# Performance work log

Hardware: AMD Instinct MI355X
Metric: run time of the kernel (lower is better)

Reference implementation:

```python
import jax, jax.numpy as jnp
import numpy as np

C = 256
G = 32            # GroupNorm groups = min(32, C)
DQK = C // 8      # q/k channel dim
EPS = 1e-5


def setup_inputs() -> dict:
    key = jax.random.key(0)
    ks = jax.random.split(key, 10)
    B, H, W = 4, 64, 64
    s = 0.02
    return {
        "x": jax.random.normal(ks[0], (B, C, H, W), dtype=jnp.float32),
        "gamma": jnp.ones((C,), jnp.float32),
        "beta": jnp.zeros((C,), jnp.float32),
        "wq": jax.random.normal(ks[1], (DQK, C), jnp.float32) * s,
        "bq": jnp.zeros((DQK,), jnp.float32),
        "wk": jax.random.normal(ks[2], (DQK, C), jnp.float32) * s,
        "bk": jnp.zeros((DQK,), jnp.float32),
        "wv": jax.random.normal(ks[3], (C, C), jnp.float32) * s,
        "bv": jnp.zeros((C,), jnp.float32),
        "wp": jax.random.normal(ks[4], (C, C), jnp.float32) * s,
        "bp": jnpp if False else jnp.zeros((C,), jnp.float32),
    }


def reference(x, gamma, beta, wq, bq, wk, bk, wv, bv, wp, bp):
    B, Cc, H, W = x.shape
    N = H * W
    # GroupNorm(32, C), affine
    h = x.reshape(B, G, Cc // G, H, W)
    mu = h.mean(axis=(2, 3, 4), keepdims=True)
    var = h.var(axis=(2, 3, 4), keepdims=True)
    h = (h - mu) * jax.lax.rsqrt(var + EPS)
    h = h.reshape(B, Cc, N) * gamma[:, None] + beta[:, None]
    # 1x1 convs == per-token linear maps over channels
    q = jnp.einsum('dc,bcn->bnd', wq, h) + bq            # [B, N, DQK]
    k = jnp.einsum('dc,bcn->bdn', wk, h) + bk[:, None]   # [B, DQK, N]
    v = jnp.einsum('ec,bcn->ben', wv, h) + bv[:, None]   # [B, C, N]
    scale = DQK ** (-0.5)
    attn = jax.nn.softmax(jnp.einsum('bnd,bdm->bnm', q, k) * scale, axis=-1)
    out = jnp.einsum('bnm,bem->ben', attn, v)            # [B, C, N]
    proj = jnp.einsum('fe,ben->bfn', wp, out) + bp[:, None]
    return x + proj.reshape(B, Cc, H, W)
```

## Files before the change

### kernel.cpp

```cpp
#include <hip/hip_runtime.h>
#include <hip/hip_bf16.h>

#define NB 4
#define CD 256
#define NT 4096
#define DQ 32

typedef __attribute__((ext_vector_type(8))) __bf16 bf16x8;
typedef __attribute__((ext_vector_type(16))) float float16v;
typedef __attribute__((ext_vector_type(4))) unsigned int uint4v;
typedef __attribute__((ext_vector_type(2))) unsigned int uint2v;

#if __has_builtin(__builtin_amdgcn_exp2f)
#define EXP2(x) __builtin_amdgcn_exp2f(x)
#else
#define EXP2(x) exp2f(x)
#endif

__device__ inline unsigned short f2bf(float f) {
  unsigned u = __float_as_uint(f);
  u += 0x7fffu + ((u >> 16) & 1u);
  return (unsigned short)(u >> 16);
}

#define BARRIER() asm volatile("s_waitcnt lgkmcnt(0)\n\ts_barrier" ::: "memory")

__global__ __launch_bounds__(1024) void gn_fused(
    const float* __restrict__ x, const float* __restrict__ gamma,
    const float* __restrict__ beta, const float* __restrict__ wq,
    const float* __restrict__ wk, const float* __restrict__ wv,
    const float* __restrict__ wp, const float* __restrict__ bq,
    const float* __restrict__ bk, const float* __restrict__ bv,
    unsigned short* __restrict__ h, unsigned short* __restrict__ wqkv,
    unsigned short* __restrict__ wpb, float* __restrict__ bias) {
  int bx = blockIdx.x;
  int tid = threadIdx.x;
  if (bx < 128) {
    int b = bx >> 5, g = bx & 31, c0 = g * 8;
    const float4* xp = (const float4*)(x + (size_t)bx * 32768);
    float va[32];
    float s = 0.f, ss = 0.f;
#pragma unroll
    for (int i = 0; i < 8; i++) {
      float4 t4 = xp[i * 1024 + tid];
      va[4 * i + 0] = t4.x;
      va[4 * i + 1] = t4.y;
      va[4 * i + 2] = t4.z;
      va[4 * i + 3] = t4.w;
      s += t4.x + t4.y + t4.z + t4.w;
      ss += t4.x * t4.x + t4.y * t4.y + t4.z * t4.z + t4.w * t4.w;
    }
#pragma unroll
    for (int off = 32; off >= 1; off >>= 1) {
      s += __shfl_xor(s, off);
      ss += __shfl_xor(ss, off);
    }
    __shared__ float red[32];
    int wid = tid >> 6;
    if ((tid & 63) == 0) {
      red[wid] = s;
      red[16 + wid] = ss;
    }
    __syncthreads();
    float S = 0.f, SS = 0.f;
#pragma unroll
    for (int i = 0; i < 16; i++) {
      S += red[i];
      SS += red[16 + i];
    }
    float mu = S * (1.f / 32768.f);
    float rstd = rsqrtf(SS * (1.f / 32768.f) - mu * mu + 1e-5f);
    float gam[8], bet[8];
#pragma unroll
    for (int i = 0; i < 8; i++) {
      gam[i] = gamma[c0 + i] * rstd;
      bet[i] = beta[c0 + i] - mu * gamma[c0 + i] * rstd;
    }
    unsigned short* hb = h + (size_t)b * NT * CD + c0;
#pragma unroll
    for (int j = 0; j < 4; j++) {
      unsigned short hv[8];
#pragma unroll
      for (int i = 0; i < 8; i++) {
        hv[i] = f2bf(va[4 * i + j] * gam[i] + bet[i]);
      }
      *(uint4v*)(hb + (size_t)(4 * tid + j) * CD) = *(uint4v*)hv;
    }
  } else {
    const float scale2 = 0.2550348909867343f;
    int i = (bx - 128) * 1024 + tid;
    if (i < 320 * 256) {
      int j = i >> 8, c = i & 255;
      float v;
      if (j < 32) v = wq[j * 256 + c] * scale2;
      else if (j < 64) v = wk[(j - 32) * 256 + c];
      else v = wv[(j - 64) * 256 + c];
      wqkv[i] = f2bf(v);
    } else if (i < 320 * 256 + 256 * 256) {
      int k = i - 320 * 256;
      wpb[k] = f2bf(wp[k]);
    } else if (i < 320 * 256 + 256 * 256 + 320) {
      int j = i - (320 * 256 + 256 * 256);
      float v;
      if (j < 32) v = bq[j] * scale2;
      else if (j < 64) v = bk[j - 32];
      else v = bv[j - 64];
      bias[j] = v;
    }
  }
}

__global__ __launch_bounds__(256) void qkv_gemm(
    const unsigned short* __restrict__ A, const unsigned short* __restrict__ H,
    const float* __restrict__ bias, unsigned short* __restrict__ qk,
    unsigned short* __restrict__ v) {
  int nt = blockIdx.x, mt = blockIdx.y, b = blockIdx.z;
  int tid = threadIdx.x, lane = tid & 63;
  int w = tid >> 6, mi = w & 1, ni = w >> 1;
  int l31 = lane & 31, hh = lane >> 5;
  int m_base = mt * 64 + 32 * mi;
  int n_base = nt * 128 + 64 * ni;
  const unsigned short* Arow = A + (size_t)(m_base + l31) * 256 + 8 * hh;
  const unsigned short* Hb = H + (size_t)b * NT * CD;
  const unsigned short* h0 = Hb + (size_t)(n_base + l31) * CD + 8 * hh;
  const unsigned short* h1 = h0 + (size_t)32 * CD;
  float16v acc0, acc1;
#pragma unroll
  for (int r = 0; r < 16; r++) { acc0[r] = 0.f; acc1[r] = 0.f; }
#pragma unroll
  for (int s = 0; s < 16; s++) {
    bf16x8 af = *(const bf16x8*)(Arow + 16 * s);
    bf16x8 b0 = *(const bf16x8*)(h0 + 16 * s);
    bf16x8 b1 = *(const bf16x8*)(h1 + 16 * s);
    acc0 = __builtin_amdgcn_mfma_f32_32x32x16_bf16(af, b0, acc0, 0, 0, 0);
    acc1 = __builtin_amdgcn_mfma_f32_32x32x16_bf16(af, b1, acc1, 0, 0, 0);
  }
  float bj[16];
  int jr[16];
#pragma unroll
  for (int r = 0; r < 16; r++) {
    jr[r] = m_base + (r & 3) + 8 * (r >> 2) + 4 * hh;
    bj[r] = bias[jr[r]];
  }
#pragma unroll
  for (int half = 0; half < 2; half++) {
    int n = n_base + 32 * half + l31;
#pragma unroll
    for (int r = 0; r < 16; r++) {
      float val = (half ? acc1[r] : acc0[r]) + bj[r];
      int j = jr[r];
      if (j < 64) {
        qk[((size_t)b * NT + n) * 64 + j] = f2bf(val);
      } else {
        int e = j - 64;
        int itg = n >> 6, sp = (n >> 4) & 3;
        int ls = ((n >> 3) & 1) * 32 + (e & 31);
        int el = n & 7, et = e >> 5;
        v[((((size_t)b * 64 + itg) * 8 + et) * 4 + sp) * 512 + ls * 8 + el] =
            f2bf(val);
      }
    }
  }
}

#define K_STAGE(PCUR)                                                         \
  if (tid >= 256) {                                                           \
    *(uint4v*)&Ks[(((PCUR) + 1) & 1) * 2304 + skr * 36 + skc] = kreg;         \
    int pk_ = (PCUR) + 2 <= 31 ? (PCUR) + 2 : 31;                             \
    kreg =                                                                    \
        *(const uint4v*)&qkb[(size_t)(mbase + pk_ * 64 + skr) * 64 + 32 + skc]; \
  }

#define QK_STEP(PCUR)                                                         \
  if (w < 4) {                                                                \
    float16v st;                                                              \
    _Pragma("unroll") for (int r = 0; r < 16; r++) st[r] = 0.f;               \
    __builtin_amdgcn_s_setprio(1);                                            \
    _Pragma("unroll") for (int s = 0; s < 2; s++) {                           \
      bf16x8 af = *(const bf16x8*)&Ks[((PCUR) & 1) * 2304 +                   \
                                      (32 * ks2 + l31) * 36 + 16 * s + 8 * hh]; \
      st = __builtin_amdgcn_mfma_f32_32x32x16_bf16(af, qfr[s], st, 0, 0, 0);  \
    }                                                                         \
    __builtin_amdgcn_s_setprio(0);                                            \
    _Pragma("unroll") for (int rq = 0; rq < 4; rq++) {                        \
      float e0 = EXP2(st[4 * rq + 0]);                                        \
      float e1 = EXP2(st[4 * rq + 1]);                                        \
      float e2 = EXP2(st[4 * rq + 2]);                                        \
      float e3 = EXP2(st[4 * rq + 3]);                                        \
      lsum += (e0 + e1) + (e2 + e3);                                          \
      uint2v pw;                                                              \
      pw[0] = __builtin_amdgcn_perm(__float_as_uint(e1), __float_as_uint(e0), \
                                    0x07060302u);                             \
      pw[1] = __builtin_amdgcn_perm(__float_as_uint(e3), __float_as_uint(e2), \
                                    0x07060302u);                             \
      *(uint2v*)&Pbuf[((PCUR) & 1) * 4352 + (qs * 32 + l31) * 68 + 8 * rq +   \
                      4 * hh + 32 * ks2] = pw;                                \
    }                                                                         \
  }

#define PV_STEP(PPREV, CURV)                                                  \
  {                                                                           \
    __builtin_amdgcn_s_setprio(1);                                            \
    _Pragma("unroll") for (int sp = 0; sp < 4; sp++) {                        \
      bf16x8 a0 = *(const bf16x8*)&Pbuf[((PPREV) & 1) * 4352 + l31 * 68 +     \
                                        16 * sp + 8 * hh];                    \
      bf16x8 a1 = *(const bf16x8*)&Pbuf[((PPREV) & 1) * 4352 +                \
                                        (32 + l31) * 68 + 16 * sp + 8 * hh];  \
      acc[0] = __builtin_amdgcn_mfma_f32_32x32x16_bf16(a0, CURV[sp], acc[0],  \
                                                       0, 0, 0);              \
      acc[1] = __builtin_amdgcn_mfma_f32_32x32x16_bf16(a1, CURV[sp], acc[1],  \
                                                       0, 0, 0);              \
    }                                                                         \
    __builtin_amdgcn_s_setprio(0);                                            \
  }

#define V_LOAD(DST, ITX)                                                      \
  {                                                                           \
    const unsigned short* vp_ = vbase + (size_t)(ITX)*16384;                  \
    _Pragma("unroll") for (int u = 0; u < 4; u++)                             \
        DST[u] = *(const bf16x8*)(vp_ + u * 512);                             \
  }

__global__ __launch_bounds__(512, 4) void attn_fused(
    const unsigned short* __restrict__ qk, const unsigned short* __restrict__ Vp,
    unsigned short* __restrict__ Pa, unsigned short* __restrict__ Pb,
    float* __restrict__ lp4) {
  int L = blockIdx.x;
  int xv = L & 7;
  int b = xv >> 1;
  int kh = xv & 1;
  int n0 = (L >> 3) * 64;
  int tid = threadIdx.x, lane = tid & 63, w = tid >> 6;
  int l31 = lane & 31, hh = lane >> 5;
  int qs = w & 1, ks2 = (w >> 1) & 1;

  __shared__ unsigned short Ks[2 * 2304];
  __shared__ unsigned short Pbuf[2 * 4352];

  const unsigned short* qkb = qk + (size_t)b * NT * 64;
  const unsigned short* vit = Vp + ((size_t)b * 64 + kh * 32) * 16384;
  const unsigned short* vbase = vit + (size_t)w * 4 * 512 + lane * 8;

  bf16x8 qfr[2];
  if (w < 4) {
    int n_g = n0 + 32 * qs + l31;
    qfr[0] = *(const bf16x8*)&qkb[(size_t)n_g * 64 + 8 * hh];
    qfr[1] = *(const bf16x8*)&qkb[(size_t)n_g * 64 + 8 * hh + 16];
  }

  int tK = tid - 256;
  int skr = tK >> 2, skc = (tK & 3) * 8;
  int mbase = kh * 2048;
  uint4v kreg;

  float16v acc[2];
#pragma unroll
  for (int q2 = 0; q2 < 2; q2++)
#pragma unroll
    for (int r = 0; r < 16; r++) acc[q2][r] = 0.f;
  float lsum = 0.f;

  bf16x8 vA[4], vB[4];
  V_LOAD(vA, 0);
  if (tid >= 256) {
    kreg = *(const uint4v*)&qkb[(size_t)(mbase + skr) * 64 + 32 + skc];
    *(uint4v*)&Ks[skr * 36 + skc] = kreg;
    kreg = *(const uint4v*)&qkb[(size_t)(mbase + 64 + skr) * 64 + 32 + skc];
  }
  BARRIER();

  K_STAGE(0);
  QK_STEP(0);
  V_LOAD(vB, 1);
  BARRIER();

  for (int p = 1; p < 31; p += 2) {
    K_STAGE(p);
    QK_STEP(p);
    PV_STEP(p - 1, vA);
    V_LOAD(vA, p + 1);
    BARRIER();
    K_STAGE(p + 1);
    QK_STEP(p + 1);
    PV_STEP(p, vB);
    V_LOAD(vB, p + 2);
    BARRIER();
  }
  QK_STEP(31);
  PV_STEP(30, vA);
  BARRIER();
  PV_STEP(31, vB);

  if (w < 4) {
    lsum += __shfl_xor(lsum, 32);
    if (hh == 0) {
      lp4[(size_t)((kh * 2 + ks2) * NB + b) * NT + n0 + 32 * qs + l31] = lsum;
    }
  }

  unsigned short* Pout = (kh ? Pb : Pa) + (size_t)b * NT * CD;
#pragma unroll
  for (int r = 0; r < 16; r++) {
    int nl = (r & 3) + 8 * (r >> 2) + 4 * hh;
    Pout[(size_t)(n0 + nl) * CD + 32 * w + l31] = f2bf(acc[0][r]);
    Pout[(size_t)(n0 + 32 + nl) * CD + 32 * w + l31] = f2bf(acc[1][r]);
  }
}

__device__ inline bf16x8 combine_frag(const unsigned short* p0,
                                      const unsigned short* p1, float inv) {
  uint4v ua = *(const uint4v*)p0;
  uint4v ub = *(const uint4v*)p1;
  uint4v r;
#pragma unroll
  for (int j = 0; j < 4; j++) {
    float lo = __uint_as_float(ua[j] << 16) + __uint_as_float(ub[j] << 16);
    float hi = __uint_as_float(ua[j] & 0xffff0000u) +
               __uint_as_float(ub[j] & 0xffff0000u);
    lo *= inv;
    hi *= inv;
    r[j] = __builtin_amdgcn_perm(__float_as_uint(hi), __float_as_uint(lo),
                                 0x07060302u);
  }
  return *(bf16x8*)&r;
}

__global__ __launch_bounds__(256) void proj_gemm(
    const unsigned short* __restrict__ Wp, const unsigned short* __restrict__ Pa,
    const unsigned short* __restrict__ Pb, const float* __restrict__ lp4,
    const float* __restrict__ bp, const float* __restrict__ x,
    float* __restrict__ out) {
  int nt = blockIdx.x, mt = blockIdx.y, b = blockIdx.z;
  int tid = threadIdx.x, lane = tid & 63;
  int w = tid >> 6, mi = w & 1, ni = w >> 1;
  int l31 = lane & 31, hh = lane >> 5;
  int m_base = mt * 64 + 32 * mi;
  int n_base = nt * 128 + 64 * ni;
  const unsigned short* Arow = Wp + (size_t)(m_base + l31) * 256 + 8 * hh;
  int nA = n_base + l31, nB = nA + 32;
  float lA = 0.f, lB = 0.f;
#pragma unroll
  for (int s4 = 0; s4 < 4; s4++) {
    lA += lp4[(size_t)(s4 * NB + b) * NT + nA];
    lB += lp4[(size_t)(s4 * NB + b) * NT + nB];
  }
  float invA = 1.f / lA, invB = 1.f / lB;
  const unsigned short* a0 = Pa + ((size_t)b * NT + nA) * CD + 8 * hh;
  const unsigned short* a1 = Pa + ((size_t)b * NT + nB) * CD + 8 * hh;
  const unsigned short* c0 = Pb + ((size_t)b * NT + nA) * CD + 8 * hh;
  const unsigned short* c1 = Pb + ((size_t)b * NT + nB) * CD + 8 * hh;
  float16v acc0, acc1;
#pragma unroll
  for (int r = 0; r < 16; r++) { acc0[r] = 0.f; acc1[r] = 0.f; }
#pragma unroll
  for (int s = 0; s < 16; s++) {
    bf16x8 af = *(const bf16x8*)(Arow + 16 * s);
    bf16x8 b0 = combine_frag(a0 + 16 * s, c0 + 16 * s, invA);
    bf16x8 b1 = combine_frag(a1 + 16 * s, c1 + 16 * s, invB);
    acc0 = __builtin_amdgcn_mfma_f32_32x32x16_bf16(af, b0, acc0, 0, 0, 0);
    acc1 = __builtin_amdgcn_mfma_f32_32x32x16_bf16(af, b1, acc1, 0, 0, 0);
  }
#pragma unroll
  for (int half = 0; half < 2; half++) {
    int n = n_base + 32 * half + l31;
#pragma unroll
    for (int r = 0; r < 16; r++) {
      int f = m_base + (r & 3) + 8 * (r >> 2) + 4 * hh;
      size_t idx = ((size_t)b * CD + f) * NT + n;
      out[idx] = x[idx] + (half ? acc1[r] : acc0[r]) + bp[f];
    }
  }
}

extern "C" void kernel_launch(void* const* d_in, const int* in_sizes, int n_in,
                              void* d_out, int out_size, void* d_ws,
                              size_t ws_size, hipStream_t stream) {
  (void)in_sizes; (void)n_in; (void)out_size; (void)ws_size;
  const float* x = (const float*)d_in[0];
  const float* gamma = (const float*)d_in[1];
  const float* beta = (const float*)d_in[2];
  const float* wq = (const float*)d_in[3];
  const float* bq = (const float*)d_in[4];
  const float* wk = (const float*)d_in[5];
  const float* bk = (const float*)d_in[6];
  const float* wv = (const float*)d_in[7];
  const float* bv = (const float*)d_in[8];
  const float* wp = (const float*)d_in[9];
  const float* bp = (const float*)d_in[10];
  float* out = (float*)d_out;

  char* ws = (char*)d_ws;
  unsigned short* h_ws = (unsigned short*)ws;
  unsigned short* qk_ws = (unsigned short*)(ws + 8388608);
  unsigned short* v_ws = (unsigned short*)(ws + 10485760);
  unsigned short* o_ws = (unsigned short*)(ws + 18874368);
  unsigned short* wqkv_b = (unsigned short*)(ws + 27262976);
  unsigned short* wp_b = (unsigned short*)(ws + 27426816);
  float* bias_q = (float*)(ws + 27557888);
  float* lp4 = (float*)(ws + 27563264);

  gn_fused<<<273, 1024, 0, stream>>>(x, gamma, beta, wq, wk, wv, wp, bq, bk,
                                     bv, h_ws, wqkv_b, wp_b, bias_q);
  dim3 gq(32, 5, NB);
  qkv_gemm<<<gq, 256, 0, stream>>>(wqkv_b, h_ws, bias_q, qk_ws, v_ws);
  attn_fused<<<512, 512, 0, stream>>>(qk_ws, v_ws, h_ws, o_ws, lp4);
  dim3 gp(32, 4, NB);
  proj_gemm<<<gp, 256, 0, stream>>>(wp_b, h_ws, o_ws, lp4, bp, x, out);
}
```

Baseline: 185.7 us.

## Stage GEMM B-operand tiles in LDS for qkv and proj kernels

Both the qkv and projection GEMMs now cooperatively load a 64-token tile of the activation operand into padded shared memory once per block, and waves read MFMA B fragments from LDS. Before, every wave read those fragments straight from global memory. In proj_gemm the two-partial combine and softmax normalisation happen once per element during staging, so they are no longer repeated across the M-tile blocks. The tile shapes change to match: qkv uses 64-token tiles with one accumulator per wave, and proj uses 128-row M tiles, with adjusted grids. This adds a barrier, LDS usage and more blocks in exchange for fewer redundant global loads.

```diff
diff --git a/kernel.cpp b/kernel.cpp
--- a/kernel.cpp
+++ b/kernel.cpp
@@ -116,49 +116,48 @@
     unsigned short* __restrict__ v) {
   int nt = blockIdx.x, mt = blockIdx.y, b = blockIdx.z;
   int tid = threadIdx.x, lane = tid & 63;
-  int w = tid >> 6, mi = w & 1, ni = w >> 1;
+  int w = tid >> 6, mi = w & 1, nq = w >> 1;
   int l31 = lane & 31, hh = lane >> 5;
+  int n0 = nt * 64;
   int m_base = mt * 64 + 32 * mi;
-  int n_base = nt * 128 + 64 * ni;
+
+  __shared__ unsigned short Hs[64 * 260];
+  const unsigned short* Hb = H + (size_t)b * NT * CD;
+#pragma unroll
+  for (int u = 0; u < 8; u++) {
+    int idx = u * 256 + tid;
+    int row = idx >> 5, col = (idx & 31) * 8;
+    *(uint4v*)&Hs[row * 260 + col] =
+        *(const uint4v*)&Hb[(size_t)(n0 + row) * CD + col];
+  }
+  __syncthreads();
+
   const unsigned short* Arow = A + (size_t)(m_base + l31) * 256 + 8 * hh;
-  const unsigned short* Hb = H + (size_t)b * NT * CD;
-  const unsigned short* h0 = Hb + (size_t)(n_base + l31) * CD + 8 * hh;
-  const unsigned short* h1 = h0 + (size_t)32 * CD;
-  float16v acc0, acc1;
-#pragma unroll
-  for (int r = 0; r < 16; r++) { acc0[r] = 0.f; acc1[r] = 0.f; }
+  const unsigned short* Brow = &Hs[(nq * 32 + l31) * 260 + 8 * hh];
+  float16v acc;
+#pragma unroll
+  for (int r = 0; r < 16; r++) acc[r] = 0.f;
 #pragma unroll
   for (int s = 0; s < 16; s++) {
     bf16x8 af = *(const bf16x8*)(Arow + 16 * s);
-    bf16x8 b0 = *(const bf16x8*)(h0 + 16 * s);
-    bf16x8 b1 = *(const bf16x8*)(h1 + 16 * s);
-    acc0 = __builtin_amdgcn_mfma_f32_32x32x16_bf16(af, b0, acc0, 0, 0, 0);
-    acc1 = __builtin_amdgcn_mfma_f32_32x32x16_bf16(af, b1, acc1, 0, 0, 0);
-  }
-  float bj[16];
-  int jr[16];
+    bf16x8 bf = *(const bf16x8*)(Brow + 16 * s);
+    acc = __builtin_amdgcn_mfma_f32_32x32x16_bf16(af, bf, acc, 0, 0, 0);
+  }
+  int n = n0 + nq * 32 + l31;
+  int itg = n >> 6, sp = (n >> 4) & 3;
+  int lsn = ((n >> 3) & 1) * 32;
+  int el = n & 7;
 #pragma unroll
   for (int r = 0; r < 16; r++) {
-    jr[r] = m_base + (r & 3) + 8 * (r >> 2) + 4 * hh;
-    bj[r] = bias[jr[r]];
-  }
-#pragma unroll
-  for (int half = 0; half < 2; half++) {
-    int n = n_base + 32 * half + l31;
-#pragma unroll
-    for (int r = 0; r < 16; r++) {
-      float val = (half ? acc1[r] : acc0[r]) + bj[r];
-      int j = jr[r];
-      if (j < 64) {
-        qk[((size_t)b * NT + n) * 64 + j] = f2bf(val);
-      } else {
-        int e = j - 64;
-        int itg = n >> 6, sp = (n >> 4) & 3;
-        int ls = ((n >> 3) & 1) * 32 + (e & 31);
-        int el = n & 7, et = e >> 5;
-        v[((((size_t)b * 64 + itg) * 8 + et) * 4 + sp) * 512 + ls * 8 + el] =
-            f2bf(val);
-      }
+    int j = m_base + (r & 3) + 8 * (r >> 2) + 4 * hh;
+    float val = acc[r] + bias[j];
+    if (j < 64) {
+      qk[((size_t)b * NT + n) * 64 + j] = f2bf(val);
+    } else {
+      int e = j - 64;
+      int et = e >> 5;
+      v[((((size_t)b * 64 + itg) * 8 + et) * 4 + sp) * 512 + (lsn + (e & 31)) * 8 +
+        el] = f2bf(val);
     }
   }
 }
@@ -307,67 +306,68 @@
   }
 }
 
-__device__ inline bf16x8 combine_frag(const unsigned short* p0,
-                                      const unsigned short* p1, float inv) {
-  uint4v ua = *(const uint4v*)p0;
-  uint4v ub = *(const uint4v*)p1;
-  uint4v r;
-#pragma unroll
-  for (int j = 0; j < 4; j++) {
-    float lo = __uint_as_float(ua[j] << 16) + __uint_as_float(ub[j] << 16);
-    float hi = __uint_as_float(ua[j] & 0xffff0000u) +
-               __uint_as_float(ub[j] & 0xffff0000u);
-    lo *= inv;
-    hi *= inv;
-    r[j] = __builtin_amdgcn_perm(__float_as_uint(hi), __float_as_uint(lo),
-                                 0x07060302u);
-  }
-  return *(bf16x8*)&r;
-}
-
 __global__ __launch_bounds__(256) void proj_gemm(
     const unsigned short* __restrict__ Wp, const unsigned short* __restrict__ Pa,
     const unsigned short* __restrict__ Pb, const float* __restrict__ lp4,
     const float* __restrict__ bp, const float* __restrict__ x,
     float* __restrict__ out) {
-  int nt = blockIdx.x, mt = blockIdx.y, b = blockIdx.z;
+  int nt = blockIdx.x, mh = blockIdx.y, b = blockIdx.z;
   int tid = threadIdx.x, lane = tid & 63;
-  int w = tid >> 6, mi = w & 1, ni = w >> 1;
+  int w = tid >> 6;
   int l31 = lane & 31, hh = lane >> 5;
-  int m_base = mt * 64 + 32 * mi;
-  int n_base = nt * 128 + 64 * ni;
+  int n0 = nt * 64;
+
+  __shared__ unsigned short Bs[64 * 260];
+  int r0 = tid >> 5, colb = (tid & 31) * 8;
+#pragma unroll
+  for (int u = 0; u < 8; u++) {
+    int row = r0 + 8 * u;
+    float lA = 0.f;
+#pragma unroll
+    for (int s4 = 0; s4 < 4; s4++)
+      lA += lp4[(size_t)(s4 * NB + b) * NT + n0 + row];
+    float inv = 1.f / lA;
+    size_t goff = ((size_t)b * NT + n0 + row) * CD + colb;
+    uint4v ua = *(const uint4v*)(Pa + goff);
+    uint4v ub = *(const uint4v*)(Pb + goff);
+    uint4v rr;
+#pragma unroll
+    for (int j = 0; j < 4; j++) {
+      float lo = __uint_as_float(ua[j] << 16) + __uint_as_float(ub[j] << 16);
+      float hi = __uint_as_float(ua[j] & 0xffff0000u) +
+                 __uint_as_float(ub[j] & 0xffff0000u);
+      lo *= inv;
+      hi *= inv;
+      rr[j] = __builtin_amdgcn_perm(__float_as_uint(hi), __float_as_uint(lo),
+                                    0x07060302u);
+    }
+    *(uint4v*)&Bs[row * 260 + colb] = rr;
+  }
+  __syncthreads();
+
+  int m_base = mh * 128 + w * 32;
   const unsigned short* Arow = Wp + (size_t)(m_base + l31) * 256 + 8 * hh;
-  int nA = n_base + l31, nB = nA + 32;
-  float lA = 0.f, lB = 0.f;
-#pragma unroll
-  for (int s4 = 0; s4 < 4; s4++) {
-    lA += lp4[(size_t)(s4 * NB + b) * NT + nA];
-    lB += lp4[(size_t)(s4 * NB + b) * NT + nB];
-  }
-  float invA = 1.f / lA, invB = 1.f / lB;
-  const unsigned short* a0 = Pa + ((size_t)b * NT + nA) * CD + 8 * hh;
-  const unsigned short* a1 = Pa + ((size_t)b * NT + nB) * CD + 8 * hh;
-  const unsigned short* c0 = Pb + ((size_t)b * NT + nA) * CD + 8 * hh;
-  const unsigned short* c1 = Pb + ((size_t)b * NT + nB) * CD + 8 * hh;
+  const unsigned short* b0p = &Bs[l31 * 260 + 8 * hh];
+  const unsigned short* b1p = &Bs[(32 + l31) * 260 + 8 * hh];
   float16v acc0, acc1;
 #pragma unroll
   for (int r = 0; r < 16; r++) { acc0[r] = 0.f; acc1[r] = 0.f; }
 #pragma unroll
   for (int s = 0; s < 16; s++) {
     bf16x8 af = *(const bf16x8*)(Arow + 16 * s);
-    bf16x8 b0 = combine_frag(a0 + 16 * s, c0 + 16 * s, invA);
-    bf16x8 b1 = combine_frag(a1 + 16 * s, c1 + 16 * s, invB);
-    acc0 = __builtin_amdgcn_mfma_f32_32x32x16_bf16(af, b0, acc0, 0, 0, 0);
-    acc1 = __builtin_amdgcn_mfma_f32_32x32x16_bf16(af, b1, acc1, 0, 0, 0);
-  }
-#pragma unroll
-  for (int half = 0; half < 2; half++) {
-    int n = n_base + 32 * half + l31;
+    bf16x8 bf0 = *(const bf16x8*)(b0p + 16 * s);
+    bf16x8 bf1 = *(const bf16x8*)(b1p + 16 * s);
+    acc0 = __builtin_amdgcn_mfma_f32_32x32x16_bf16(af, bf0, acc0, 0, 0, 0);
+    acc1 = __builtin_amdgcn_mfma_f32_32x32x16_bf16(af, bf1, acc1, 0, 0, 0);
+  }
+#pragma unroll
+  for (int nq = 0; nq < 2; nq++) {
+    int n = n0 + nq * 32 + l31;
 #pragma unroll
     for (int r = 0; r < 16; r++) {
       int f = m_base + (r & 3) + 8 * (r >> 2) + 4 * hh;
       size_t idx = ((size_t)b * CD + f) * NT + n;
-      out[idx] = x[idx] + (half ? acc1[r] : acc0[r]) + bp[f];
+      out[idx] = x[idx] + (nq ? acc1[r] : acc0[r]) + bp[f];
     }
   }
 }
@@ -401,9 +401,9 @@
 
   gn_fused<<<273, 1024, 0, stream>>>(x, gamma, beta, wq, wk, wv, wp, bq, bk,
                                      bv, h_ws, wqkv_b, wp_b, bias_q);
-  dim3 gq(32, 5, NB);
+  dim3 gq(64, 5, NB);
   qkv_gemm<<<gq, 256, 0, stream>>>(wqkv_b, h_ws, bias_q, qk_ws, v_ws);
   attn_fused<<<512, 512, 0, stream>>>(qk_ws, v_ws, h_ws, o_ws, lp4);
-  dim3 gp(32, 4, NB);
+  dim3 gp(64, 2, NB);
   proj_gemm<<<gp, 256, 0, stream>>>(wp_b, h_ws, o_ws, lp4, bp, x, out);
 }
```

Result: slower. 189.9 us (+2.3%).
